# Kernel optimization log

Hardware: AMD Instinct MI355X
Metric: run time of the kernel (lower is better)

Reference implementation:

```python
import jax, jax.numpy as jnp
import numpy as np

B, N, D, H = 2, 2048, 1024, 16
DH = D // H  # 64


def setup_inputs() -> dict:
    key = jax.random.key(0)
    k1, k2, k3, k4, k5 = jax.random.split(key, 5)
    x = jax.random.normal(k1, (B, N, D), dtype=jnp.float32)
    # per-head kqv Linear weights, stacked: [H, D, 3*DH] (acts as x @ W)
    W_kqv = jax.random.normal(k2, (H, D, 3 * DH), dtype=jnp.float32) * 0.02
    b_kqv = jax.random.normal(k3, (H, 3 * DH), dtype=jnp.float32) * 0.02
    W_proj = jax.random.normal(k4, (D, D), dtype=jnp.float32) * 0.02
    b_proj = jax.random.normal(k5, (D,), dtype=jnp.float32) * 0.02
    return {"x": x, "W_kqv": W_kqv, "b_kqv": b_kqv, "W_proj": W_proj, "b_proj": b_proj}


def reference(x, W_kqv, b_kqv, W_proj, b_proj):
    # per-head projections, all heads batched: [B, H, N, 3*DH]
    kqv = jnp.einsum('bnd,hde->bhne', x, W_kqv) + b_kqv[None, :, None, :]
    # original chunk order is k, q, v
    k, q, v = jnp.split(kqv, 3, axis=-1)  # each [B, H, N, DH]
    # scores: A = q @ k^T / sqrt(DH)  -> [B, H, N, N]
    A = jnp.einsum('bhnd,bhmd->bhnm', q, k) / jnp.sqrt(jnp.asarray(DH, x.dtype))
    causal = jnp.tril(jnp.ones((N, N), dtype=bool))
    A = jnp.where(causal[None, None, :, :], A, -jnp.inf)
    attn = jax.nn.softmax(A, axis=-1)
    sa = jnp.einsum('bhnm,bhmd->bhnd', attn, v)          # [B, H, N, DH]
    sa = sa.transpose(0, 2, 1, 3).reshape(B, N, D)        # concat heads
    out = sa @ W_proj.T + b_proj                          # output projection
    return out
```

## Files before the change

### kernel.cpp

```cpp
#include <hip/hip_runtime.h>
#include <hip/hip_bf16.h>
#include <cstdint>
#include <cstddef>

#define B_  2
#define N_  2048
#define D_  1024
#define H_  16
#define DH_ 64
#define E3_ 192

typedef __attribute__((ext_vector_type(8))) short short8;
typedef __attribute__((ext_vector_type(8))) unsigned short ushort8v;
typedef __attribute__((ext_vector_type(4))) float floatx4;

static __device__ __forceinline__ unsigned short f2bf(float f) {
  union { float f; unsigned u; } c; c.f = f;
  unsigned r = c.u + 0x7fffu + ((c.u >> 16) & 1u);
  return (unsigned short)(r >> 16);
}

#define MFMA(a,b,c) __builtin_amdgcn_mfma_f32_16x16x32_bf16((a),(b),(c),0,0,0)

#define GL_LDS16(g, l) __builtin_amdgcn_global_load_lds( \
    (const __attribute__((address_space(1))) void*)(g),  \
    (__attribute__((address_space(3))) void*)(l), 16, 0, 0)

__global__ __launch_bounds__(256) void k_prep(const float* __restrict__ x,
                                              const float* __restrict__ Wkqv,
                                              const float* __restrict__ Wproj,
                                              unsigned short* __restrict__ Xb,
                                              unsigned short* __restrict__ Wt,
                                              unsigned short* __restrict__ Wpb) {
  __shared__ float tile[64][65];
  int bx = blockIdx.x, t = threadIdx.x;
  if (bx < 2048 || bx >= 2816) {
    const float* in = (bx < 2048) ? x : Wproj;
    unsigned short* out = (bx < 2048) ? Xb : Wpb;
    int i = ((bx < 2048) ? bx : bx - 2816) * 256 + t;
    const float4* p = (const float4*)in + (size_t)i * 2;
    float4 a = p[0], b = p[1];
    ushort8v o;
    o[0]=f2bf(a.x); o[1]=f2bf(a.y); o[2]=f2bf(a.z); o[3]=f2bf(a.w);
    o[4]=f2bf(b.x); o[5]=f2bf(b.y); o[6]=f2bf(b.z); o[7]=f2bf(b.w);
    *((ushort8v*)out + i) = o;
    return;
  }
  int idx = bx - 2048;
  int d0 = (idx & 15) * 64, rem = idx >> 4;
  int cat = rem % 3, h = rem / 3, e0 = cat * 64;
  const float* Wp = Wkqv + (size_t)h * D_ * E3_;
  int dr = t >> 2, ec = (t & 3) * 16;
#pragma unroll
  for (int j = 0; j < 16; j += 4) {
    float4 wv = *(const float4*)&Wp[(size_t)(d0 + dr) * E3_ + e0 + ec + j];
    tile[dr][ec + j + 0] = wv.x; tile[dr][ec + j + 1] = wv.y;
    tile[dr][ec + j + 2] = wv.z; tile[dr][ec + j + 3] = wv.w;
  }
  __syncthreads();
  int er = t >> 2, dc = (t & 3) * 16;
  ushort8v o0, o1;
#pragma unroll
  for (int j = 0; j < 8; j++) o0[j] = f2bf(tile[dc + j][er]);
#pragma unroll
  for (int j = 0; j < 8; j++) o1[j] = f2bf(tile[dc + 8 + j][er]);
  size_t o = ((size_t)(cat * 1024 + h * 64 + er)) * D_ + d0 + dc;
  *(ushort8v*)&Wt[o]     = o0;
  *(ushort8v*)&Wt[o + 8] = o1;
}

__global__ __launch_bounds__(512, 2) void k_qkv(const unsigned short* __restrict__ Xb,
                                                const unsigned short* __restrict__ Wt,
                                                const float* __restrict__ bkqv,
                                                unsigned short* __restrict__ Qb,
                                                unsigned short* __restrict__ Kb,
                                                unsigned short* __restrict__ Vt) {
  __shared__ unsigned short LDSf[65536];
  const int t = threadIdx.x;
  const int wid = t >> 6, lane = t & 63, quad = lane >> 4, l16 = lane & 15;
  const int wr = wid >> 2, wc = wid & 3;
  const int m0 = blockIdx.x * 256, c0 = blockIdx.y * 256;

  floatx4 acc[8][4];
#pragma unroll
  for (int i = 0; i < 8; i++)
#pragma unroll
    for (int j = 0; j < 4; j++) acc[i][j] = (floatx4){0.f, 0.f, 0.f, 0.f};

  const int slr = t >> 3;
  const int sco = ((t & 7) ^ (slr & 7)) * 8;
  const unsigned short* gA0 = Xb + (size_t)(m0 +   0 + slr) * D_ + sco;
  const unsigned short* gA1 = Xb + (size_t)(m0 +  64 + slr) * D_ + sco;
  const unsigned short* gA2 = Xb + (size_t)(m0 + 128 + slr) * D_ + sco;
  const unsigned short* gA3 = Xb + (size_t)(m0 + 192 + slr) * D_ + sco;
  const unsigned short* gB0 = Wt + (size_t)(c0 +   0 + slr) * D_ + sco;
  const unsigned short* gB1 = Wt + (size_t)(c0 +  64 + slr) * D_ + sco;
  const unsigned short* gB2 = Wt + (size_t)(c0 + 128 + slr) * D_ + sco;
  const unsigned short* gB3 = Wt + (size_t)(c0 + 192 + slr) * D_ + sco;
#define SA(gp, q, s, bb) GL_LDS16((gp) + (s) * 64, &LDSf[(bb) * 16384 + (q) * 4096 + t * 8])
#define SB(gp, q, s, bb) GL_LDS16((gp) + (s) * 64, &LDSf[32768 + (bb) * 16384 + (q) * 4096 + t * 8])

  const int aoff0 = ((quad)     ^ (l16 & 7)) * 8;
  const int aoff1 = ((4 + quad) ^ (l16 & 7)) * 8;
  const unsigned short* Abase = &LDSf[(wr * 128 + l16) * 64];
  const unsigned short* Bbase = &LDSf[32768 + (wc * 64 + l16) * 64];

  SA(gA0, 0, 0, 0); SA(gA1, 1, 0, 0); SA(gA2, 2, 0, 0); SA(gA3, 3, 0, 0);
  SB(gB0, 0, 0, 0); SB(gB1, 1, 0, 0); SB(gB2, 2, 0, 0); SB(gB3, 3, 0, 0);
  SA(gA0, 0, 1, 1); SA(gA2, 2, 1, 1);
  asm volatile("s_waitcnt vmcnt(2)" ::: "memory");
  __builtin_amdgcn_s_barrier();

  for (int s = 0; s < 16; s++) {
    const int buf = s & 1, nbuf = buf ^ 1;
    const int so = buf * 16384;
    short8 a[4][2], b[4][2];
#pragma unroll
    for (int mi = 0; mi < 4; mi++) {
      a[mi][0] = *(const short8*)&Abase[so + mi * 1024 + aoff0];
      a[mi][1] = *(const short8*)&Abase[so + mi * 1024 + aoff1];
    }
#pragma unroll
    for (int ni = 0; ni < 2; ni++) {
      b[ni][0] = *(const short8*)&Bbase[so + ni * 1024 + aoff0];
      b[ni][1] = *(const short8*)&Bbase[so + ni * 1024 + aoff1];
    }
    if (s < 15) {
      SA(gA1, 1, s + 1, nbuf); SA(gA3, 3, s + 1, nbuf);
      SB(gB0, 0, s + 1, nbuf); SB(gB1, 1, s + 1, nbuf);
      SB(gB2, 2, s + 1, nbuf); SB(gB3, 3, s + 1, nbuf);
    }
    __builtin_amdgcn_s_barrier();
    asm volatile("s_waitcnt lgkmcnt(0)" ::: "memory");
    __builtin_amdgcn_sched_barrier(0);
    __builtin_amdgcn_s_setprio(1);
#pragma unroll
    for (int mi = 0; mi < 4; mi++)
#pragma unroll
      for (int ni = 0; ni < 2; ni++) {
        acc[mi][ni] = MFMA(a[mi][0], b[ni][0], acc[mi][ni]);
        acc[mi][ni] = MFMA(a[mi][1], b[ni][1], acc[mi][ni]);
      }
    __builtin_amdgcn_s_setprio(0);
    __builtin_amdgcn_s_barrier();
#pragma unroll
    for (int ni = 2; ni < 4; ni++) {
      b[ni][0] = *(const short8*)&Bbase[so + ni * 1024 + aoff0];
      b[ni][1] = *(const short8*)&Bbase[so + ni * 1024 + aoff1];
    }
    __builtin_amdgcn_s_barrier();
    asm volatile("s_waitcnt lgkmcnt(0)" ::: "memory");
    __builtin_amdgcn_sched_barrier(0);
    __builtin_amdgcn_s_setprio(1);
#pragma unroll
    for (int mi = 0; mi < 4; mi++)
#pragma unroll
      for (int ni = 2; ni < 4; ni++) {
        acc[mi][ni] = MFMA(a[mi][0], b[ni][0], acc[mi][ni]);
        acc[mi][ni] = MFMA(a[mi][1], b[ni][1], acc[mi][ni]);
      }
    __builtin_amdgcn_s_setprio(0);
    __builtin_amdgcn_s_barrier();
#pragma unroll
    for (int mi = 0; mi < 4; mi++) {
      a[mi][0] = *(const short8*)&Abase[so + (mi + 4) * 1024 + aoff0];
      a[mi][1] = *(const short8*)&Abase[so + (mi + 4) * 1024 + aoff1];
    }
    if (s < 14) { SA(gA0, 0, s + 2, buf); SA(gA2, 2, s + 2, buf); }
    __builtin_amdgcn_s_barrier();
    asm volatile("s_waitcnt lgkmcnt(0)" ::: "memory");
    __builtin_amdgcn_sched_barrier(0);
    __builtin_amdgcn_s_setprio(1);
#pragma unroll
    for (int mi = 0; mi < 4; mi++)
#pragma unroll
      for (int ni = 0; ni < 2; ni++) {
        acc[mi + 4][ni] = MFMA(a[mi][0], b[ni][0], acc[mi + 4][ni]);
        acc[mi + 4][ni] = MFMA(a[mi][1], b[ni][1], acc[mi + 4][ni]);
      }
    __builtin_amdgcn_s_setprio(0);
    __builtin_amdgcn_s_barrier();
    __builtin_amdgcn_s_setprio(1);
#pragma unroll
    for (int mi = 0; mi < 4; mi++)
#pragma unroll
      for (int ni = 2; ni < 4; ni++) {
        acc[mi + 4][ni] = MFMA(a[mi][0], b[ni][0], acc[mi + 4][ni]);
        acc[mi + 4][ni] = MFMA(a[mi][1], b[ni][1], acc[mi + 4][ni]);
      }
    __builtin_amdgcn_s_setprio(0);
    if (s < 14) { asm volatile("s_waitcnt vmcnt(2)" ::: "memory"); }
    else        { asm volatile("s_waitcnt vmcnt(0)" ::: "memory"); }
    __builtin_amdgcn_s_barrier();
  }

  __syncthreads();
  unsigned short* scr = &LDSf[wid * 8192];
  const int cat = c0 >> 10;
  const int h   = ((c0 + wc * 64) >> 6) & 15;
  const int bb  = (m0 + wr * 128) >> 11;
  const int n0b = (m0 + wr * 128) & (N_ - 1);
  const int l8 = lane & 7, lh = lane >> 3;
  if (cat < 2) {
    const float scale = (cat == 1) ? 0.18033688011112042f : 1.0f;
    float bias[4];
#pragma unroll
    for (int ni = 0; ni < 4; ni++) bias[ni] = bkqv[h * E3_ + cat * 64 + ni * 16 + l16];
#pragma unroll
    for (int mi = 0; mi < 8; mi++)
#pragma unroll
      for (int ni = 0; ni < 4; ni++)
#pragma unroll
        for (int r = 0; r < 4; r++) {
          int rl = mi * 16 + quad * 4 + r, cl = ni * 16 + l16;
          scr[rl * 64 + ((((cl >> 3) ^ rl) & 7) * 8) + (cl & 7)] =
              f2bf((acc[mi][ni][r] + bias[ni]) * scale);
        }
    asm volatile("s_waitcnt lgkmcnt(0)" ::: "memory");
    unsigned short* dst = (cat == 0) ? Kb : Qb;
#pragma unroll
    for (int j = 0; j < 16; j++) {
      int rl = j * 8 + lh;
      short8 vv = *(const short8*)&scr[rl * 64 + ((l8 ^ lh) * 8)];
      *(short8*)&dst[((size_t)(bb * H_ + h) * N_ + n0b + rl) * DH_ + l8 * 8] = vv;
    }
  } else {
    float bias[4];
#pragma unroll
    for (int ni = 0; ni < 4; ni++) bias[ni] = bkqv[h * E3_ + 128 + ni * 16 + l16];
#pragma unroll
    for (int mi = 0; mi < 8; mi++)
#pragma unroll
      for (int ni = 0; ni < 4; ni++)
#pragma unroll
        for (int r = 0; r < 4; r++) {
          int nl = mi * 16 + quad * 4 + r, e = ni * 16 + l16;
          scr[e * 128 + ((((nl >> 3) ^ e) & 15) * 8) + (nl & 7)] =
              f2bf(acc[mi][ni][r] + bias[ni]);
        }
    asm volatile("s_waitcnt lgkmcnt(0)" ::: "memory");
#pragma unroll
    for (int j = 0; j < 16; j++) {
      int e = (j & 7) * 8 + lh;
      int nc = l8 + (j >> 3) * 8;
      short8 vv = *(const short8*)&scr[e * 128 + (((nc ^ e) & 15) * 8)];
      *(short8*)&Vt[((size_t)(bb * H_ + h) * DH_ + e) * N_ + n0b + nc * 8] = vv;
    }
  }
#undef SA
#undef SB
}

__global__ __launch_bounds__(256) void k_flash(const unsigned short* __restrict__ Qb,
                                               const unsigned short* __restrict__ Kb,
                                               const unsigned short* __restrict__ Vt,
                                               unsigned short* __restrict__ sab) {
  int bh = blockIdx.x;
  int yr = blockIdx.y, g = yr >> 3, o = yr & 7;
  int qb = (g == 0) ? o : (g == 1) ? 31 - o : (g == 2) ? 8 + o : 23 - o;
  int q0b = qb * 64;
  int wave = threadIdx.x >> 6;
  int lane = threadIdx.x & 63, quad = lane >> 4, l16 = lane & 15;
  const unsigned short* Qp = Qb + (size_t)bh * N_ * DH_;
  const unsigned short* Kp = Kb + (size_t)bh * N_ * DH_;
  const unsigned short* Vp = Vt + (size_t)bh * DH_ * N_;
  __shared__ unsigned short Klds[2][2 * 64 * 32];
  __shared__ unsigned short Vlds[2][2 * 64 * 32];
  __shared__ unsigned short Plds[4][16 * 64];
  unsigned short* P = Plds[wave];

  int q0w = q0b + wave * 16;
  short8 qf0 = *(const short8*)&Qp[(q0w + l16) * DH_ + quad * 8];
  short8 qf1 = *(const short8*)&Qp[(q0w + l16) * DH_ + 32 + quad * 8];

  int swz = ((lane & 3) ^ ((lane >> 3) & 3)) * 8;
  const unsigned short* gK = Kp + (size_t)(wave * 16 + (lane >> 2)) * DH_ + swz;
  const unsigned short* gV = Vp + (size_t)(wave * 16 + (lane >> 2)) * N_ + swz;
  int lofs = (wave * 16) * 32;
  int xr = ((l16 >> 1) & 3) * 8;
  int pxr = l16 & 7;

#define FSTAGE(ii, bb) do {                                              \
    size_t ko_ = (size_t)(ii) * 64 * DH_; int vo_ = (ii) * 64;           \
    GL_LDS16(gK + ko_,      &Klds[bb][lofs]);                            \
    GL_LDS16(gK + ko_ + 32, &Klds[bb][lofs + 64 * 32]);                  \
    GL_LDS16(gV + vo_,      &Vlds[bb][lofs]);                            \
    GL_LDS16(gV + vo_ + 32, &Vlds[bb][lofs + 64 * 32]);                  \
  } while (0)

  floatx4 O[4];
  float lr = 0.f;
#pragma unroll
  for (int r = 0; r < 4; r++) O[r] = (floatx4){0.f, 0.f, 0.f, 0.f};

  int nt = (q0b >> 6) + 1;
  FSTAGE(0, 0);
  if (nt > 1) FSTAGE(1, 1);

  for (int i = 0; i < nt; i++) {
    int buf = i & 1;
    if (i + 1 < nt) { asm volatile("s_waitcnt vmcnt(4)" ::: "memory"); }
    else            { asm volatile("s_waitcnt vmcnt(0)" ::: "memory"); }
    __builtin_amdgcn_s_barrier();
    __builtin_amdgcn_sched_barrier(0);
    short8 kf[4][2], vf[4][2];
#pragma unroll
    for (int c = 0; c < 4; c++) {
      kf[c][0] = *(const short8*)&Klds[buf][(c * 16 + l16) * 32 + ((quad * 8) ^ xr)];
      kf[c][1] = *(const short8*)&Klds[buf][(64 + c * 16 + l16) * 32 + ((quad * 8) ^ xr)];
      vf[c][0] = *(const short8*)&Vlds[buf][(c * 16 + l16) * 32 + ((quad * 8) ^ xr)];
      vf[c][1] = *(const short8*)&Vlds[buf][(64 + c * 16 + l16) * 32 + ((quad * 8) ^ xr)];
    }
    floatx4 s[4];
    __builtin_amdgcn_s_setprio(1);
#pragma unroll
    for (int c = 0; c < 4; c++) {
      s[c] = (floatx4){0.f, 0.f, 0.f, 0.f};
      s[c] = MFMA(kf[c][0], qf0, s[c]);
      s[c] = MFMA(kf[c][1], qf1, s[c]);
    }
    __builtin_amdgcn_s_setprio(0);
    if (i == nt - 1) {
#pragma unroll
      for (int c = 0; c < 4; c++)
#pragma unroll
        for (int r = 0; r < 4; r++) {
          int key = c * 16 + quad * 4 + r;
          if (key > wave * 16 + l16) s[c][r] = -1e30f;
        }
    }
#pragma unroll
    for (int c = 0; c < 4; c++)
#pragma unroll
      for (int r = 0; r < 4; r++)
        s[c][r] = __builtin_amdgcn_exp2f(s[c][r]);
#pragma unroll
    for (int c = 0; c < 4; c++)
      lr += (s[c][0] + s[c][1]) + (s[c][2] + s[c][3]);
#pragma unroll
    for (int c = 0; c < 4; c++) {
      unsigned plo = (unsigned)f2bf(s[c][0]) | ((unsigned)f2bf(s[c][1]) << 16);
      unsigned phi = (unsigned)f2bf(s[c][2]) | ((unsigned)f2bf(s[c][3]) << 16);
      int ch = c * 2 + (quad >> 1);
      uint2 pk; pk.x = plo; pk.y = phi;
      *(uint2*)&P[l16 * 64 + ((ch ^ pxr) * 8) + (quad & 1) * 4] = pk;
    }
    __asm__ volatile("s_waitcnt lgkmcnt(0)" ::: "memory");
    short8 pa0 = *(const short8*)&P[l16 * 64 + ((quad ^ pxr) * 8)];
    short8 pa1 = *(const short8*)&P[l16 * 64 + (((quad + 4) ^ pxr) * 8)];
    __asm__ volatile("" ::: "memory");
    __builtin_amdgcn_s_setprio(1);
#pragma unroll
    for (int dt = 0; dt < 4; dt++) {
      O[dt] = MFMA(pa0, vf[dt][0], O[dt]);
      O[dt] = MFMA(pa1, vf[dt][1], O[dt]);
    }
    __builtin_amdgcn_s_setprio(0);
    __builtin_amdgcn_s_barrier();
    __builtin_amdgcn_sched_barrier(0);
    if (i + 2 < nt) FSTAGE(i + 2, buf);
  }
#undef FSTAGE

  lr += __shfl_xor(lr, 16);
  lr += __shfl_xor(lr, 32);

  int b = bh >> 4, h = bh & 15;
#pragma unroll
  for (int r = 0; r < 4; r++) {
    float inv = 1.0f / __shfl(lr, quad * 4 + r);
    size_t base = ((size_t)b * N_ + q0w + quad * 4 + r) * D_ + h * DH_;
#pragma unroll
    for (int dt = 0; dt < 4; dt++) sab[base + dt * 16 + l16] = f2bf(O[dt][r] * inv);
  }
}

__global__ __launch_bounds__(512) void k_proj(const unsigned short* __restrict__ sab,
                                              const unsigned short* __restrict__ Wpb,
                                              const float* __restrict__ bproj,
                                              float* __restrict__ out) {
  __shared__ unsigned short LDSp[32768];
  const int t = threadIdx.x;
  const int wid = t >> 6, lane = t & 63, quad = lane >> 4, l16 = lane & 15;
  const int wr = wid >> 1, wc = wid & 1;
  const int bid = blockIdx.x;
  const int m0 = (bid >> 3) * 128, c0 = (bid & 7) * 128;

  floatx4 acc[2][4];
#pragma unroll
  for (int i = 0; i < 2; i++)
#pragma unroll
    for (int j = 0; j < 4; j++) acc[i][j] = (floatx4){0.f, 0.f, 0.f, 0.f};

  const int slr = t >> 3;
  const int sco = ((t & 7) ^ (slr & 7)) * 8;
  const unsigned short* gA0 = sab + (size_t)(m0 +  0 + slr) * D_ + sco;
  const unsigned short* gA1 = sab + (size_t)(m0 + 64 + slr) * D_ + sco;
  const unsigned short* gB0 = Wpb + (size_t)(c0 +  0 + slr) * D_ + sco;
  const unsigned short* gB1 = Wpb + (size_t)(c0 + 64 + slr) * D_ + sco;
#define PA(gp, q, s, bb) GL_LDS16((gp) + (s) * 64, &LDSp[(bb) * 8192 + (q) * 4096 + t * 8])
#define PB(gp, q, s, bb) GL_LDS16((gp) + (s) * 64, &LDSp[16384 + (bb) * 8192 + (q) * 4096 + t * 8])

  const int aoff0 = ((quad)     ^ (l16 & 7)) * 8;
  const int aoff1 = ((4 + quad) ^ (l16 & 7)) * 8;
  const unsigned short* Abase = &LDSp[(wr * 32 + l16) * 64];
  const unsigned short* Bbase = &LDSp[16384 + (wc * 64 + l16) * 64];

  PA(gA0, 0, 0, 0); PA(gA1, 1, 0, 0); PB(gB0, 0, 0, 0); PB(gB1, 1, 0, 0);
  PA(gA0, 0, 1, 1); PA(gA1, 1, 1, 1); PB(gB0, 0, 1, 1); PB(gB1, 1, 1, 1);

  for (int i = 0; i < 16; i++) {
    const int buf = i & 1;
    const int so = buf * 8192;
    if (i + 1 < 16) { asm volatile("s_waitcnt vmcnt(4)" ::: "memory"); }
    else            { asm volatile("s_waitcnt vmcnt(0)" ::: "memory"); }
    __builtin_amdgcn_s_barrier();
    __builtin_amdgcn_sched_barrier(0);
    short8 a[2][2], b[4][2];
#pragma unroll
    for (int mi = 0; mi < 2; mi++) {
      a[mi][0] = *(const short8*)&Abase[so + mi * 1024 + aoff0];
      a[mi][1] = *(const short8*)&Abase[so + mi * 1024 + aoff1];
    }
#pragma unroll
    for (int ni = 0; ni < 4; ni++) {
      b[ni][0] = *(const short8*)&Bbase[so + ni * 1024 + aoff0];
      b[ni][1] = *(const short8*)&Bbase[so + ni * 1024 + aoff1];
    }
    __builtin_amdgcn_s_setprio(1);
#pragma unroll
    for (int mi = 0; mi < 2; mi++)
#pragma unroll
      for (int ni = 0; ni < 4; ni++) {
        acc[mi][ni] = MFMA(a[mi][0], b[ni][0], acc[mi][ni]);
        acc[mi][ni] = MFMA(a[mi][1], b[ni][1], acc[mi][ni]);
      }
    __builtin_amdgcn_s_setprio(0);
    __builtin_amdgcn_s_barrier();
    __builtin_amdgcn_sched_barrier(0);
    if (i + 2 < 16) {
      PA(gA0, 0, i + 2, buf); PA(gA1, 1, i + 2, buf);
      PB(gB0, 0, i + 2, buf); PB(gB1, 1, i + 2, buf);
    }
  }

#pragma unroll
  for (int mi = 0; mi < 2; mi++)
#pragma unroll
    for (int ni = 0; ni < 4; ni++) {
      int col = c0 + wc * 64 + ni * 16 + l16;
      int grow = m0 + wr * 32 + mi * 16 + quad * 4;
      float bias = bproj[col];
#pragma unroll
      for (int r = 0; r < 4; r++)
        out[(size_t)(grow + r) * D_ + col] = acc[mi][ni][r] + bias;
    }
#undef PA
#undef PB
}

extern "C" void kernel_launch(void* const* d_in, const int* in_sizes, int n_in,
                              void* d_out, int out_size, void* d_ws, size_t ws_size,
                              hipStream_t stream) {
  const float* x     = (const float*)d_in[0];
  const float* Wkqv  = (const float*)d_in[1];
  const float* bkqv  = (const float*)d_in[2];
  const float* Wproj = (const float*)d_in[3];
  const float* bproj = (const float*)d_in[4];
  float* out = (float*)d_out;

  char* w = (char*)d_ws;
  unsigned short* Xb  = (unsigned short*)(w);
  unsigned short* Wt  = (unsigned short*)(w + (8u  << 20));
  unsigned short* Wpb = (unsigned short*)(w + (14u << 20));
  unsigned short* Qb  = (unsigned short*)(w + (16u << 20));
  unsigned short* Kb  = (unsigned short*)(w + (24u << 20));
  unsigned short* Vt  = (unsigned short*)(w + (32u << 20));
  unsigned short* sa  = (unsigned short*)(w + (40u << 20));

  k_prep<<<2048 + 768 + 512, 256, 0, stream>>>(x, Wkqv, Wproj, Xb, Wt, Wpb);
  k_qkv<<<dim3(B_ * N_ / 256, 3072 / 256), 512, 0, stream>>>(Xb, Wt, bkqv, Qb, Kb, Vt);
  k_flash<<<dim3(B_ * H_, N_ / 64), 256, 0, stream>>>(Qb, Kb, Vt, sa);
  k_proj<<<(B_ * N_ / 128) * (D_ / 128), 512, 0, stream>>>(sa, Wpb, bproj, out);
}
```

Baseline: 168.7 us.

## Triple-buffer output projection LDS and interleave loads with split MFMA phases

```diff
diff --git a/kernel.cpp b/kernel.cpp
--- a/kernel.cpp
+++ b/kernel.cpp
@@ -379,7 +379,7 @@
                                               const unsigned short* __restrict__ Wpb,
                                               const float* __restrict__ bproj,
                                               float* __restrict__ out) {
-  __shared__ unsigned short LDSp[32768];
+  __shared__ unsigned short LDSp[49152];
   const int t = threadIdx.x;
   const int wid = t >> 6, lane = t & 63, quad = lane >> 4, l16 = lane & 15;
   const int wr = wid >> 1, wc = wid & 1;
@@ -399,23 +399,22 @@
   const unsigned short* gB0 = Wpb + (size_t)(c0 +  0 + slr) * D_ + sco;
   const unsigned short* gB1 = Wpb + (size_t)(c0 + 64 + slr) * D_ + sco;
 #define PA(gp, q, s, bb) GL_LDS16((gp) + (s) * 64, &LDSp[(bb) * 8192 + (q) * 4096 + t * 8])
-#define PB(gp, q, s, bb) GL_LDS16((gp) + (s) * 64, &LDSp[16384 + (bb) * 8192 + (q) * 4096 + t * 8])
+#define PB(gp, q, s, bb) GL_LDS16((gp) + (s) * 64, &LDSp[24576 + (bb) * 8192 + (q) * 4096 + t * 8])
 
   const int aoff0 = ((quad)     ^ (l16 & 7)) * 8;
   const int aoff1 = ((4 + quad) ^ (l16 & 7)) * 8;
   const unsigned short* Abase = &LDSp[(wr * 32 + l16) * 64];
-  const unsigned short* Bbase = &LDSp[16384 + (wc * 64 + l16) * 64];
+  const unsigned short* Bbase = &LDSp[24576 + (wc * 64 + l16) * 64];
 
   PA(gA0, 0, 0, 0); PA(gA1, 1, 0, 0); PB(gB0, 0, 0, 0); PB(gB1, 1, 0, 0);
   PA(gA0, 0, 1, 1); PA(gA1, 1, 1, 1); PB(gB0, 0, 1, 1); PB(gB1, 1, 1, 1);
-
-  for (int i = 0; i < 16; i++) {
-    const int buf = i & 1;
+  asm volatile("s_waitcnt vmcnt(4)" ::: "memory");
+  __builtin_amdgcn_s_barrier();
+
+#pragma unroll
+  for (int s = 0; s < 16; s++) {
+    const int buf = s % 3, nb2 = (s + 2) % 3;
     const int so = buf * 8192;
-    if (i + 1 < 16) { asm volatile("s_waitcnt vmcnt(4)" ::: "memory"); }
-    else            { asm volatile("s_waitcnt vmcnt(0)" ::: "memory"); }
-    __builtin_amdgcn_s_barrier();
-    __builtin_amdgcn_sched_barrier(0);
     short8 a[2][2], b[4][2];
 #pragma unroll
     for (int mi = 0; mi < 2; mi++) {
@@ -423,25 +422,45 @@
       a[mi][1] = *(const short8*)&Abase[so + mi * 1024 + aoff1];
     }
 #pragma unroll
-    for (int ni = 0; ni < 4; ni++) {
+    for (int ni = 0; ni < 2; ni++) {
       b[ni][0] = *(const short8*)&Bbase[so + ni * 1024 + aoff0];
       b[ni][1] = *(const short8*)&Bbase[so + ni * 1024 + aoff1];
     }
+    if (s + 2 < 16) { PA(gA0, 0, s + 2, nb2); PA(gA1, 1, s + 2, nb2); }
+    __builtin_amdgcn_s_barrier();
+    asm volatile("s_waitcnt lgkmcnt(0)" ::: "memory");
+    __builtin_amdgcn_sched_barrier(0);
     __builtin_amdgcn_s_setprio(1);
 #pragma unroll
     for (int mi = 0; mi < 2; mi++)
 #pragma unroll
-      for (int ni = 0; ni < 4; ni++) {
+      for (int ni = 0; ni < 2; ni++) {
         acc[mi][ni] = MFMA(a[mi][0], b[ni][0], acc[mi][ni]);
         acc[mi][ni] = MFMA(a[mi][1], b[ni][1], acc[mi][ni]);
       }
     __builtin_amdgcn_s_setprio(0);
     __builtin_amdgcn_s_barrier();
-    __builtin_amdgcn_sched_barrier(0);
-    if (i + 2 < 16) {
-      PA(gA0, 0, i + 2, buf); PA(gA1, 1, i + 2, buf);
-      PB(gB0, 0, i + 2, buf); PB(gB1, 1, i + 2, buf);
-    }
+#pragma unroll
+    for (int ni = 2; ni < 4; ni++) {
+      b[ni][0] = *(const short8*)&Bbase[so + ni * 1024 + aoff0];
+      b[ni][1] = *(const short8*)&Bbase[so + ni * 1024 + aoff1];
+    }
+    if (s + 2 < 16) { PB(gB0, 0, s + 2, nb2); PB(gB1, 1, s + 2, nb2); }
+    __builtin_amdgcn_s_barrier();
+    asm volatile("s_waitcnt lgkmcnt(0)" ::: "memory");
+    __builtin_amdgcn_sched_barrier(0);
+    __builtin_amdgcn_s_setprio(1);
+#pragma unroll
+    for (int mi = 0; mi < 2; mi++)
+#pragma unroll
+      for (int ni = 2; ni < 4; ni++) {
+        acc[mi][ni] = MFMA(a[mi][0], b[ni][0], acc[mi][ni]);
+        acc[mi][ni] = MFMA(a[mi][1], b[ni][1], acc[mi][ni]);
+      }
+    __builtin_amdgcn_s_setprio(0);
+    if (s <= 13)      { asm volatile("s_waitcnt vmcnt(4)" ::: "memory"); }
+    else if (s == 14) { asm volatile("s_waitcnt vmcnt(0)" ::: "memory"); }
+    __builtin_amdgcn_s_barrier();
   }
 
 #pragma unroll
```

After: 172.3 us. 1.02x slower.

## Double flash-attention query tile to 128 rows per block for K/V reuse

Applied to the files above, without the earlier changes.

```diff
diff --git a/kernel.cpp b/kernel.cpp
--- a/kernel.cpp
+++ b/kernel.cpp
@@ -256,9 +256,9 @@
                                                const unsigned short* __restrict__ Vt,
                                                unsigned short* __restrict__ sab) {
   int bh = blockIdx.x;
-  int yr = blockIdx.y, g = yr >> 3, o = yr & 7;
-  int qb = (g == 0) ? o : (g == 1) ? 31 - o : (g == 2) ? 8 + o : 23 - o;
-  int q0b = qb * 64;
+  int y = blockIdx.y, g8 = y >> 3, o = y & 7;
+  int qb = (g8 == 0) ? o : 15 - o;
+  int q0b = qb * 128;
   int wave = threadIdx.x >> 6;
   int lane = threadIdx.x & 63, quad = lane >> 4, l16 = lane & 15;
   const unsigned short* Qp = Qb + (size_t)bh * N_ * DH_;
@@ -266,12 +266,16 @@
   const unsigned short* Vp = Vt + (size_t)bh * DH_ * N_;
   __shared__ unsigned short Klds[2][2 * 64 * 32];
   __shared__ unsigned short Vlds[2][2 * 64 * 32];
-  __shared__ unsigned short Plds[4][16 * 64];
+  __shared__ unsigned short Plds[4][2 * 16 * 64];
   unsigned short* P = Plds[wave];
 
-  int q0w = q0b + wave * 16;
-  short8 qf0 = *(const short8*)&Qp[(q0w + l16) * DH_ + quad * 8];
-  short8 qf1 = *(const short8*)&Qp[(q0w + l16) * DH_ + 32 + quad * 8];
+  int q0w = q0b + wave * 32;
+  short8 qf[2][2];
+#pragma unroll
+  for (int g = 0; g < 2; g++) {
+    qf[g][0] = *(const short8*)&Qp[(q0w + g * 16 + l16) * DH_ + quad * 8];
+    qf[g][1] = *(const short8*)&Qp[(q0w + g * 16 + l16) * DH_ + 32 + quad * 8];
+  }
 
   int swz = ((lane & 3) ^ ((lane >> 3) & 3)) * 8;
   const unsigned short* gK = Kp + (size_t)(wave * 16 + (lane >> 2)) * DH_ + swz;
@@ -288,14 +292,16 @@
     GL_LDS16(gV + vo_ + 32, &Vlds[bb][lofs + 64 * 32]);                  \
   } while (0)
 
-  floatx4 O[4];
-  float lr = 0.f;
-#pragma unroll
-  for (int r = 0; r < 4; r++) O[r] = (floatx4){0.f, 0.f, 0.f, 0.f};
-
-  int nt = (q0b >> 6) + 1;
+  floatx4 O[2][4];
+  float lr[2] = {0.f, 0.f};
+#pragma unroll
+  for (int g = 0; g < 2; g++)
+#pragma unroll
+    for (int dt = 0; dt < 4; dt++) O[g][dt] = (floatx4){0.f, 0.f, 0.f, 0.f};
+
+  int nt = (q0b >> 6) + 2;
   FSTAGE(0, 0);
-  if (nt > 1) FSTAGE(1, 1);
+  FSTAGE(1, 1);
 
   for (int i = 0; i < nt; i++) {
     int buf = i & 1;
@@ -311,50 +317,61 @@
       vf[c][0] = *(const short8*)&Vlds[buf][(c * 16 + l16) * 32 + ((quad * 8) ^ xr)];
       vf[c][1] = *(const short8*)&Vlds[buf][(64 + c * 16 + l16) * 32 + ((quad * 8) ^ xr)];
     }
-    floatx4 s[4];
-    __builtin_amdgcn_s_setprio(1);
-#pragma unroll
-    for (int c = 0; c < 4; c++) {
-      s[c] = (floatx4){0.f, 0.f, 0.f, 0.f};
-      s[c] = MFMA(kf[c][0], qf0, s[c]);
-      s[c] = MFMA(kf[c][1], qf1, s[c]);
-    }
-    __builtin_amdgcn_s_setprio(0);
-    if (i == nt - 1) {
+#pragma unroll
+    for (int g = 0; g < 2; g++) {
+      floatx4 s[4];
+      __builtin_amdgcn_s_setprio(1);
+#pragma unroll
+      for (int c = 0; c < 4; c++) {
+        s[c] = (floatx4){0.f, 0.f, 0.f, 0.f};
+        s[c] = MFMA(kf[c][0], qf[g][0], s[c]);
+        s[c] = MFMA(kf[c][1], qf[g][1], s[c]);
+      }
+      __builtin_amdgcn_s_setprio(0);
+      if (i >= nt - 2) {
+        int di = i - (nt - 2);
+        int rowrel = wave * 32 + g * 16 + l16;
+#pragma unroll
+        for (int c = 0; c < 4; c++)
+#pragma unroll
+          for (int r = 0; r < 4; r++) {
+            int keyrel = di * 64 + c * 16 + quad * 4 + r;
+            if (keyrel > rowrel) s[c][r] = -1e30f;
+          }
+      }
 #pragma unroll
       for (int c = 0; c < 4; c++)
 #pragma unroll
-        for (int r = 0; r < 4; r++) {
-          int key = c * 16 + quad * 4 + r;
-          if (key > wave * 16 + l16) s[c][r] = -1e30f;
-        }
-    }
-#pragma unroll
-    for (int c = 0; c < 4; c++)
-#pragma unroll
-      for (int r = 0; r < 4; r++)
-        s[c][r] = __builtin_amdgcn_exp2f(s[c][r]);
-#pragma unroll
-    for (int c = 0; c < 4; c++)
-      lr += (s[c][0] + s[c][1]) + (s[c][2] + s[c][3]);
-#pragma unroll
-    for (int c = 0; c < 4; c++) {
-      unsigned plo = (unsigned)f2bf(s[c][0]) | ((unsigned)f2bf(s[c][1]) << 16);
-      unsigned phi = (unsigned)f2bf(s[c][2]) | ((unsigned)f2bf(s[c][3]) << 16);
-      int ch = c * 2 + (quad >> 1);
-      uint2 pk; pk.x = plo; pk.y = phi;
-      *(uint2*)&P[l16 * 64 + ((ch ^ pxr) * 8) + (quad & 1) * 4] = pk;
+        for (int r = 0; r < 4; r++)
+          s[c][r] = __builtin_amdgcn_exp2f(s[c][r]);
+#pragma unroll
+      for (int c = 0; c < 4; c++)
+        lr[g] += (s[c][0] + s[c][1]) + (s[c][2] + s[c][3]);
+#pragma unroll
+      for (int c = 0; c < 4; c++) {
+        unsigned plo = (unsigned)f2bf(s[c][0]) | ((unsigned)f2bf(s[c][1]) << 16);
+        unsigned phi = (unsigned)f2bf(s[c][2]) | ((unsigned)f2bf(s[c][3]) << 16);
+        int ch = c * 2 + (quad >> 1);
+        uint2 pk; pk.x = plo; pk.y = phi;
+        *(uint2*)&P[g * 1024 + l16 * 64 + ((ch ^ pxr) * 8) + (quad & 1) * 4] = pk;
+      }
     }
     __asm__ volatile("s_waitcnt lgkmcnt(0)" ::: "memory");
-    short8 pa0 = *(const short8*)&P[l16 * 64 + ((quad ^ pxr) * 8)];
-    short8 pa1 = *(const short8*)&P[l16 * 64 + (((quad + 4) ^ pxr) * 8)];
+    short8 pa[2][2];
+#pragma unroll
+    for (int g = 0; g < 2; g++) {
+      pa[g][0] = *(const short8*)&P[g * 1024 + l16 * 64 + ((quad ^ pxr) * 8)];
+      pa[g][1] = *(const short8*)&P[g * 1024 + l16 * 64 + (((quad + 4) ^ pxr) * 8)];
+    }
     __asm__ volatile("" ::: "memory");
     __builtin_amdgcn_s_setprio(1);
 #pragma unroll
-    for (int dt = 0; dt < 4; dt++) {
-      O[dt] = MFMA(pa0, vf[dt][0], O[dt]);
-      O[dt] = MFMA(pa1, vf[dt][1], O[dt]);
-    }
+    for (int g = 0; g < 2; g++)
+#pragma unroll
+      for (int dt = 0; dt < 4; dt++) {
+        O[g][dt] = MFMA(pa[g][0], vf[dt][0], O[g][dt]);
+        O[g][dt] = MFMA(pa[g][1], vf[dt][1], O[g][dt]);
+      }
     __builtin_amdgcn_s_setprio(0);
     __builtin_amdgcn_s_barrier();
     __builtin_amdgcn_sched_barrier(0);
@@ -362,17 +379,22 @@
   }
 #undef FSTAGE
 
-  lr += __shfl_xor(lr, 16);
-  lr += __shfl_xor(lr, 32);
+#pragma unroll
+  for (int g = 0; g < 2; g++) {
+    lr[g] += __shfl_xor(lr[g], 16);
+    lr[g] += __shfl_xor(lr[g], 32);
+  }
 
   int b = bh >> 4, h = bh & 15;
 #pragma unroll
-  for (int r = 0; r < 4; r++) {
-    float inv = 1.0f / __shfl(lr, quad * 4 + r);
-    size_t base = ((size_t)b * N_ + q0w + quad * 4 + r) * D_ + h * DH_;
-#pragma unroll
-    for (int dt = 0; dt < 4; dt++) sab[base + dt * 16 + l16] = f2bf(O[dt][r] * inv);
-  }
+  for (int g = 0; g < 2; g++)
+#pragma unroll
+    for (int r = 0; r < 4; r++) {
+      float inv = 1.0f / __shfl(lr[g], quad * 4 + r);
+      size_t base = ((size_t)b * N_ + q0w + g * 16 + quad * 4 + r) * D_ + h * DH_;
+#pragma unroll
+      for (int dt = 0; dt < 4; dt++) sab[base + dt * 16 + l16] = f2bf(O[g][dt][r] * inv);
+    }
 }
 
 __global__ __launch_bounds__(512) void k_proj(const unsigned short* __restrict__ sab,
@@ -480,6 +502,6 @@
 
   k_prep<<<2048 + 768 + 512, 256, 0, stream>>>(x, Wkqv, Wproj, Xb, Wt, Wpb);
   k_qkv<<<dim3(B_ * N_ / 256, 3072 / 256), 512, 0, stream>>>(Xb, Wt, bkqv, Qb, Kb, Vt);
-  k_flash<<<dim3(B_ * H_, N_ / 64), 256, 0, stream>>>(Qb, Kb, Vt, sa);
+  k_flash<<<dim3(B_ * H_, N_ / 128), 256, 0, stream>>>(Qb, Kb, Vt, sa);
   k_proj<<<(B_ * N_ / 128) * (D_ / 128), 512, 0, stream>>>(sa, Wpb, bproj, out);
 }
```

New measurement: 177.6 us. +5.3%, slower.

## Shrink QKV GEMM tile to 128x128 with simpler double-buffered pipeline

Applied to the files above, without the earlier changes.

```diff
diff --git a/kernel.cpp b/kernel.cpp
--- a/kernel.cpp
+++ b/kernel.cpp
@@ -69,137 +69,86 @@
   *(ushort8v*)&Wt[o + 8] = o1;
 }
 
-__global__ __launch_bounds__(512, 2) void k_qkv(const unsigned short* __restrict__ Xb,
+__global__ __launch_bounds__(256, 2) void k_qkv(const unsigned short* __restrict__ Xb,
                                                 const unsigned short* __restrict__ Wt,
                                                 const float* __restrict__ bkqv,
                                                 unsigned short* __restrict__ Qb,
                                                 unsigned short* __restrict__ Kb,
                                                 unsigned short* __restrict__ Vt) {
-  __shared__ unsigned short LDSf[65536];
+  __shared__ unsigned short LDSq[32768];
   const int t = threadIdx.x;
   const int wid = t >> 6, lane = t & 63, quad = lane >> 4, l16 = lane & 15;
-  const int wr = wid >> 2, wc = wid & 3;
-  const int m0 = blockIdx.x * 256, c0 = blockIdx.y * 256;
-
-  floatx4 acc[8][4];
-#pragma unroll
-  for (int i = 0; i < 8; i++)
+  const int wm = (wid >> 1) * 64, wn = (wid & 1) * 64;
+  const int m0 = blockIdx.x * 128, c0 = blockIdx.y * 128;
+
+  floatx4 acc[4][4];
+#pragma unroll
+  for (int i = 0; i < 4; i++)
 #pragma unroll
     for (int j = 0; j < 4; j++) acc[i][j] = (floatx4){0.f, 0.f, 0.f, 0.f};
 
   const int slr = t >> 3;
   const int sco = ((t & 7) ^ (slr & 7)) * 8;
-  const unsigned short* gA0 = Xb + (size_t)(m0 +   0 + slr) * D_ + sco;
-  const unsigned short* gA1 = Xb + (size_t)(m0 +  64 + slr) * D_ + sco;
-  const unsigned short* gA2 = Xb + (size_t)(m0 + 128 + slr) * D_ + sco;
-  const unsigned short* gA3 = Xb + (size_t)(m0 + 192 + slr) * D_ + sco;
-  const unsigned short* gB0 = Wt + (size_t)(c0 +   0 + slr) * D_ + sco;
-  const unsigned short* gB1 = Wt + (size_t)(c0 +  64 + slr) * D_ + sco;
-  const unsigned short* gB2 = Wt + (size_t)(c0 + 128 + slr) * D_ + sco;
-  const unsigned short* gB3 = Wt + (size_t)(c0 + 192 + slr) * D_ + sco;
-#define SA(gp, q, s, bb) GL_LDS16((gp) + (s) * 64, &LDSf[(bb) * 16384 + (q) * 4096 + t * 8])
-#define SB(gp, q, s, bb) GL_LDS16((gp) + (s) * 64, &LDSf[32768 + (bb) * 16384 + (q) * 4096 + t * 8])
+  const unsigned short* gA0 = Xb + (size_t)(m0 +  0 + slr) * D_ + sco;
+  const unsigned short* gA1 = Xb + (size_t)(m0 + 32 + slr) * D_ + sco;
+  const unsigned short* gA2 = Xb + (size_t)(m0 + 64 + slr) * D_ + sco;
+  const unsigned short* gA3 = Xb + (size_t)(m0 + 96 + slr) * D_ + sco;
+  const unsigned short* gB0 = Wt + (size_t)(c0 +  0 + slr) * D_ + sco;
+  const unsigned short* gB1 = Wt + (size_t)(c0 + 32 + slr) * D_ + sco;
+  const unsigned short* gB2 = Wt + (size_t)(c0 + 64 + slr) * D_ + sco;
+  const unsigned short* gB3 = Wt + (size_t)(c0 + 96 + slr) * D_ + sco;
+#define SA(qq, s, bb) GL_LDS16(gA##qq + (s) * 64, &LDSq[(bb) * 8192 + (qq) * 2048 + t * 8])
+#define SB(qq, s, bb) GL_LDS16(gB##qq + (s) * 64, &LDSq[16384 + (bb) * 8192 + (qq) * 2048 + t * 8])
+#define STAGE(s, bb) do { SA(0,s,bb); SA(1,s,bb); SA(2,s,bb); SA(3,s,bb); \
+                          SB(0,s,bb); SB(1,s,bb); SB(2,s,bb); SB(3,s,bb); } while (0)
 
   const int aoff0 = ((quad)     ^ (l16 & 7)) * 8;
   const int aoff1 = ((4 + quad) ^ (l16 & 7)) * 8;
-  const unsigned short* Abase = &LDSf[(wr * 128 + l16) * 64];
-  const unsigned short* Bbase = &LDSf[32768 + (wc * 64 + l16) * 64];
-
-  SA(gA0, 0, 0, 0); SA(gA1, 1, 0, 0); SA(gA2, 2, 0, 0); SA(gA3, 3, 0, 0);
-  SB(gB0, 0, 0, 0); SB(gB1, 1, 0, 0); SB(gB2, 2, 0, 0); SB(gB3, 3, 0, 0);
-  SA(gA0, 0, 1, 1); SA(gA2, 2, 1, 1);
-  asm volatile("s_waitcnt vmcnt(2)" ::: "memory");
-  __builtin_amdgcn_s_barrier();
-
-  for (int s = 0; s < 16; s++) {
-    const int buf = s & 1, nbuf = buf ^ 1;
-    const int so = buf * 16384;
+
+  STAGE(0, 0);
+  STAGE(1, 1);
+
+  for (int i = 0; i < 16; i++) {
+    const int buf = i & 1;
+    const int soA = buf * 8192, soB = 16384 + buf * 8192;
+    if (i + 1 < 16) { asm volatile("s_waitcnt vmcnt(8)" ::: "memory"); }
+    else            { asm volatile("s_waitcnt vmcnt(0)" ::: "memory"); }
+    __builtin_amdgcn_s_barrier();
+    __builtin_amdgcn_sched_barrier(0);
     short8 a[4][2], b[4][2];
 #pragma unroll
     for (int mi = 0; mi < 4; mi++) {
-      a[mi][0] = *(const short8*)&Abase[so + mi * 1024 + aoff0];
-      a[mi][1] = *(const short8*)&Abase[so + mi * 1024 + aoff1];
-    }
-#pragma unroll
-    for (int ni = 0; ni < 2; ni++) {
-      b[ni][0] = *(const short8*)&Bbase[so + ni * 1024 + aoff0];
-      b[ni][1] = *(const short8*)&Bbase[so + ni * 1024 + aoff1];
-    }
-    if (s < 15) {
-      SA(gA1, 1, s + 1, nbuf); SA(gA3, 3, s + 1, nbuf);
-      SB(gB0, 0, s + 1, nbuf); SB(gB1, 1, s + 1, nbuf);
-      SB(gB2, 2, s + 1, nbuf); SB(gB3, 3, s + 1, nbuf);
-    }
-    __builtin_amdgcn_s_barrier();
-    asm volatile("s_waitcnt lgkmcnt(0)" ::: "memory");
-    __builtin_amdgcn_sched_barrier(0);
+      a[mi][0] = *(const short8*)&LDSq[soA + (wm + mi * 16 + l16) * 64 + aoff0];
+      a[mi][1] = *(const short8*)&LDSq[soA + (wm + mi * 16 + l16) * 64 + aoff1];
+    }
+#pragma unroll
+    for (int ni = 0; ni < 4; ni++) {
+      b[ni][0] = *(const short8*)&LDSq[soB + (wn + ni * 16 + l16) * 64 + aoff0];
+      b[ni][1] = *(const short8*)&LDSq[soB + (wn + ni * 16 + l16) * 64 + aoff1];
+    }
     __builtin_amdgcn_s_setprio(1);
 #pragma unroll
     for (int mi = 0; mi < 4; mi++)
 #pragma unroll
-      for (int ni = 0; ni < 2; ni++) {
+      for (int ni = 0; ni < 4; ni++) {
         acc[mi][ni] = MFMA(a[mi][0], b[ni][0], acc[mi][ni]);
         acc[mi][ni] = MFMA(a[mi][1], b[ni][1], acc[mi][ni]);
       }
     __builtin_amdgcn_s_setprio(0);
     __builtin_amdgcn_s_barrier();
-#pragma unroll
-    for (int ni = 2; ni < 4; ni++) {
-      b[ni][0] = *(const short8*)&Bbase[so + ni * 1024 + aoff0];
-      b[ni][1] = *(const short8*)&Bbase[so + ni * 1024 + aoff1];
-    }
-    __builtin_amdgcn_s_barrier();
-    asm volatile("s_waitcnt lgkmcnt(0)" ::: "memory");
-    __builtin_amdgcn_sched_barrier(0);
-    __builtin_amdgcn_s_setprio(1);
-#pragma unroll
-    for (int mi = 0; mi < 4; mi++)
-#pragma unroll
-      for (int ni = 2; ni < 4; ni++) {
-        acc[mi][ni] = MFMA(a[mi][0], b[ni][0], acc[mi][ni]);
-        acc[mi][ni] = MFMA(a[mi][1], b[ni][1], acc[mi][ni]);
-      }
-    __builtin_amdgcn_s_setprio(0);
-    __builtin_amdgcn_s_barrier();
-#pragma unroll
-    for (int mi = 0; mi < 4; mi++) {
-      a[mi][0] = *(const short8*)&Abase[so + (mi + 4) * 1024 + aoff0];
-      a[mi][1] = *(const short8*)&Abase[so + (mi + 4) * 1024 + aoff1];
-    }
-    if (s < 14) { SA(gA0, 0, s + 2, buf); SA(gA2, 2, s + 2, buf); }
-    __builtin_amdgcn_s_barrier();
-    asm volatile("s_waitcnt lgkmcnt(0)" ::: "memory");
-    __builtin_amdgcn_sched_barrier(0);
-    __builtin_amdgcn_s_setprio(1);
-#pragma unroll
-    for (int mi = 0; mi < 4; mi++)
-#pragma unroll
-      for (int ni = 0; ni < 2; ni++) {
-        acc[mi + 4][ni] = MFMA(a[mi][0], b[ni][0], acc[mi + 4][ni]);
-        acc[mi + 4][ni] = MFMA(a[mi][1], b[ni][1], acc[mi + 4][ni]);
-      }
-    __builtin_amdgcn_s_setprio(0);
-    __builtin_amdgcn_s_barrier();
-    __builtin_amdgcn_s_setprio(1);
-#pragma unroll
-    for (int mi = 0; mi < 4; mi++)
-#pragma unroll
-      for (int ni = 2; ni < 4; ni++) {
-        acc[mi + 4][ni] = MFMA(a[mi][0], b[ni][0], acc[mi + 4][ni]);
-        acc[mi + 4][ni] = MFMA(a[mi][1], b[ni][1], acc[mi + 4][ni]);
-      }
-    __builtin_amdgcn_s_setprio(0);
-    if (s < 14) { asm volatile("s_waitcnt vmcnt(2)" ::: "memory"); }
-    else        { asm volatile("s_waitcnt vmcnt(0)" ::: "memory"); }
-    __builtin_amdgcn_s_barrier();
-  }
+    __builtin_amdgcn_sched_barrier(0);
+    if (i + 2 < 16) STAGE(i + 2, buf);
+  }
+#undef SA
+#undef SB
+#undef STAGE
 
   __syncthreads();
-  unsigned short* scr = &LDSf[wid * 8192];
+  unsigned short* scr = &LDSq[wid * 4096];
   const int cat = c0 >> 10;
-  const int h   = ((c0 + wc * 64) >> 6) & 15;
-  const int bb  = (m0 + wr * 128) >> 11;
-  const int n0b = (m0 + wr * 128) & (N_ - 1);
+  const int h   = ((c0 + wn) >> 6) & 15;
+  const int bb  = (m0 + wm) >> 11;
+  const int n0b = (m0 + wm) & (N_ - 1);
   const int l8 = lane & 7, lh = lane >> 3;
   if (cat < 2) {
     const float scale = (cat == 1) ? 0.18033688011112042f : 1.0f;
@@ -207,19 +156,19 @@
 #pragma unroll
     for (int ni = 0; ni < 4; ni++) bias[ni] = bkqv[h * E3_ + cat * 64 + ni * 16 + l16];
 #pragma unroll
-    for (int mi = 0; mi < 8; mi++)
+    for (int mi = 0; mi < 4; mi++)
 #pragma unroll
       for (int ni = 0; ni < 4; ni++)
 #pragma unroll
         for (int r = 0; r < 4; r++) {
           int rl = mi * 16 + quad * 4 + r, cl = ni * 16 + l16;
-          scr[rl * 64 + ((((cl >> 3) ^ rl) & 7) * 8) + (cl & 7)] =
+          scr[rl * 64 + (((cl >> 3) ^ (rl & 7)) * 8) + (cl & 7)] =
               f2bf((acc[mi][ni][r] + bias[ni]) * scale);
         }
     asm volatile("s_waitcnt lgkmcnt(0)" ::: "memory");
     unsigned short* dst = (cat == 0) ? Kb : Qb;
 #pragma unroll
-    for (int j = 0; j < 16; j++) {
+    for (int j = 0; j < 8; j++) {
       int rl = j * 8 + lh;
       short8 vv = *(const short8*)&scr[rl * 64 + ((l8 ^ lh) * 8)];
       *(short8*)&dst[((size_t)(bb * H_ + h) * N_ + n0b + rl) * DH_ + l8 * 8] = vv;
@@ -229,26 +178,23 @@
 #pragma unroll
     for (int ni = 0; ni < 4; ni++) bias[ni] = bkqv[h * E3_ + 128 + ni * 16 + l16];
 #pragma unroll
-    for (int mi = 0; mi < 8; mi++)
+    for (int mi = 0; mi < 4; mi++)
 #pragma unroll
       for (int ni = 0; ni < 4; ni++)
 #pragma unroll
         for (int r = 0; r < 4; r++) {
           int nl = mi * 16 + quad * 4 + r, e = ni * 16 + l16;
-          scr[e * 128 + ((((nl >> 3) ^ e) & 15) * 8) + (nl & 7)] =
+          scr[e * 64 + (((nl >> 3) ^ (e & 7)) * 8) + (nl & 7)] =
               f2bf(acc[mi][ni][r] + bias[ni]);
         }
     asm volatile("s_waitcnt lgkmcnt(0)" ::: "memory");
 #pragma unroll
-    for (int j = 0; j < 16; j++) {
-      int e = (j & 7) * 8 + lh;
-      int nc = l8 + (j >> 3) * 8;
-      short8 vv = *(const short8*)&scr[e * 128 + (((nc ^ e) & 15) * 8)];
-      *(short8*)&Vt[((size_t)(bb * H_ + h) * DH_ + e) * N_ + n0b + nc * 8] = vv;
-    }
-  }
-#undef SA
-#undef SB
+    for (int j = 0; j < 8; j++) {
+      int le = j * 8 + lh;
+      short8 vv = *(const short8*)&scr[le * 64 + ((l8 ^ lh) * 8)];
+      *(short8*)&Vt[((size_t)(bb * H_ + h) * DH_ + le) * N_ + n0b + l8 * 8] = vv;
+    }
+  }
 }
 
 __global__ __launch_bounds__(256) void k_flash(const unsigned short* __restrict__ Qb,
@@ -479,7 +425,7 @@
   unsigned short* sa  = (unsigned short*)(w + (40u << 20));
 
   k_prep<<<2048 + 768 + 512, 256, 0, stream>>>(x, Wkqv, Wproj, Xb, Wt, Wpb);
-  k_qkv<<<dim3(B_ * N_ / 256, 3072 / 256), 512, 0, stream>>>(Xb, Wt, bkqv, Qb, Kb, Vt);
+  k_qkv<<<dim3(B_ * N_ / 128, 3072 / 128), 256, 0, stream>>>(Xb, Wt, bkqv, Qb, Kb, Vt);
   k_flash<<<dim3(B_ * H_, N_ / 64), 256, 0, stream>>>(Qb, Kb, Vt, sa);
   k_proj<<<(B_ * N_ / 128) * (D_ / 128), 512, 0, stream>>>(sa, Wpb, bproj, out);
 }
```

After: 168.4 us. About the same (-0.1%).
